# Kernel optimization log

Hardware: AMD Instinct MI355X
Metric: run time of the kernel (lower is better)

The kernel has to match this reference:

```python
import jax, jax.numpy as jnp
import numpy as np

D_MODEL = 1024
N_HEADS = 16
D_K = 64
CHUNK_LEN = 64


def setup_inputs() -> dict:
    key = jax.random.key(0)
    ks = jax.random.split(key, 10)
    B, S = 4, 2048
    NC, NN, NL = 32, 2, 128
    s = 1.0 / np.sqrt(D_MODEL)
    inp = {
        "query": jax.random.normal(ks[0], (B, S, D_MODEL), dtype=jnp.float32),
        "key": jax.random.normal(ks[1], (B, NC, NN, NL, D_MODEL), dtype=jnp.float32),
        # Linear weights stored as [in, out] (equivalent to torch W.T)
        "Wq": jax.random.normal(ks[2], (D_MODEL, N_HEADS * D_K), dtype=jnp.float32) * s,
        "bq": jnp.zeros((N_HEADS * D_K,), dtype=jnp.float32),
        "Wk": jax.random.normal(ks[3], (D_MODEL, N_HEADS * D_K), dtype=jnp.float32) * s,
        "bk": jnp.zeros((N_HEADS * D_K,), dtype=jnp.float32),
        "Wv": jax.random.normal(ks[4], (D_MODEL, N_HEADS * D_K), dtype=jnp.float32) * s,
        "bv": jnp.zeros((N_HEADS * D_K,), dtype=jnp.float32),
        "Wo": jax.random.normal(ks[5], (N_HEADS * D_K, D_MODEL), dtype=jnp.float32) * s,
        "bo": jnp.zeros((D_MODEL,), dtype=jnp.float32),
    }
    return inp


def reference(query, key, Wq, bq, Wk, bk, Wv, bv, Wo, bo):
    B, S, D = query.shape
    _, NC, NN, NL, _ = key.shape
    L = NN * NL  # kv length per chunk
    # reshape query into chunks: [B, NC, chunk_len, D]
    q_in = query.reshape(B, NC, CHUNK_LEN, D)
    kv_in = key.reshape(B, NC, L, D)  # key used for both K and V in the original
    # projections, split heads: [B, NC, H, T, d_k]
    q = (q_in @ Wq + bq).reshape(B, NC, CHUNK_LEN, N_HEADS, D_K).transpose(0, 1, 3, 2, 4)
    k = (kv_in @ Wk + bk).reshape(B, NC, L, N_HEADS, D_K).transpose(0, 1, 3, 2, 4)
    v = (kv_in @ Wv + bv).reshape(B, NC, L, N_HEADS, D_K).transpose(0, 1, 3, 2, 4)
    # attention per (batch, chunk, head)
    scores = jnp.einsum("bchqd,bchkd->bchqk", q, k) / jnp.sqrt(jnp.float32(D_K))
    attn = jax.nn.softmax(scores, axis=-1)
    o = jnp.einsum("bchqk,bchkd->bchqd", attn, v)
    # merge heads: [B, NC, chunk_len, H*d_k]
    o = o.transpose(0, 1, 3, 2, 4).reshape(B, NC, CHUNK_LEN, N_HEADS * D_K)
    out = o @ Wo + bo
    return out.reshape(B, S, D)
```

## Files before the change

### kernel.cpp

```cpp
#include <hip/hip_runtime.h>
#include <hip/hip_bf16.h>
#include <stdint.h>

#define DMODEL 1024
#define NHEADS 16
#define DK 64
#define TQ 64
#define LKV 256
#define MQ 8192
#define MKV 32768

typedef __bf16 bf16x8 __attribute__((ext_vector_type(8)));
typedef float f32x4 __attribute__((ext_vector_type(4)));
typedef unsigned short u16x8 __attribute__((ext_vector_type(8)));
typedef unsigned short u16;

__device__ __forceinline__ unsigned short f2bf(float f) {
    union { float f; unsigned int i; } x; x.f = f;
    unsigned int r = (x.i + 0x7FFFu + ((x.i >> 16) & 1u)) >> 16;
    return (unsigned short)r;
}

__device__ __forceinline__ void gload_lds16(const void* g, void* l) {
    __builtin_amdgcn_global_load_lds(
        (const __attribute__((address_space(1))) unsigned int*)g,
        (__attribute__((address_space(3))) unsigned int*)l, 16, 0, 0);
}

__global__ __launch_bounds__(256) void cvt_f32_bf16(const float* __restrict__ in,
                                                    unsigned short* __restrict__ out) {
    long long i = ((long long)blockIdx.x * 256 + threadIdx.x) * 8;
    f32x4 a = *(const f32x4*)(in + i);
    f32x4 b = *(const f32x4*)(in + i + 4);
    u16x8 o;
    o[0] = f2bf(a[0]); o[1] = f2bf(a[1]); o[2] = f2bf(a[2]); o[3] = f2bf(a[3]);
    o[4] = f2bf(b[0]); o[5] = f2bf(b[1]); o[6] = f2bf(b[2]); o[7] = f2bf(b[3]);
    *(u16x8*)(out + i) = o;
}

__global__ __launch_bounds__(256) void transpose_w_cvt4(const float* __restrict__ w0,
                                                        const float* __restrict__ w1,
                                                        const float* __restrict__ w2,
                                                        const float* __restrict__ w3,
                                                        u16* __restrict__ o0,
                                                        u16* __restrict__ o1,
                                                        u16* __restrict__ o2,
                                                        u16* __restrict__ o3) {
    __shared__ float tile[64][65];
    const float* in; u16* out;
    switch (blockIdx.z) {
        case 0: in = w0; out = o0; break;
        case 1: in = w1; out = o1; break;
        case 2: in = w2; out = o2; break;
        default: in = w3; out = o3; break;
    }
    int bi = blockIdx.y, bj = blockIdx.x;
    int tid = threadIdx.x;
    int c = tid & 63, r0 = tid >> 6;
#pragma unroll
    for (int p = 0; p < 16; ++p) {
        int r = r0 + 4 * p;
        tile[r][c] = in[(size_t)(bi * 64 + r) * 1024 + bj * 64 + c];
    }
    __syncthreads();
#pragma unroll
    for (int p = 0; p < 16; ++p) {
        int r = r0 + 4 * p;
        out[(size_t)(bj * 64 + r) * 1024 + bi * 64 + c] = f2bf(tile[c][r]);
    }
}

template <int OUTMODE>
__global__ __launch_bounds__(256) void gemm_bias(const u16* __restrict__ A,
                                                 const u16* __restrict__ Bt,
                                                 const float* __restrict__ bias,
                                                 void* __restrict__ OutV) {
    __shared__ alignas(16) u16 aLds[128 * 32];
    __shared__ alignas(16) u16 bLds[128 * 32];

    int tid = threadIdx.x;
    int lane = tid & 63, wid = tid >> 6;
    int m0 = blockIdx.x * 128;
    int n0 = blockIdx.y * 128;
    int wr = (wid >> 1) * 64, wc = (wid & 1) * 64;

    f32x4 zero = {0.f, 0.f, 0.f, 0.f};
    f32x4 acc[4][4];
#pragma unroll
    for (int i = 0; i < 4; ++i)
#pragma unroll
        for (int j = 0; j < 4; ++j) acc[i][j] = zero;

    int sr = lane >> 2;
    int sk = (lane & 3) * 8;
    const u16* aG = A + (size_t)(m0 + sr) * 1024 + sk;
    const u16* bG = Bt + (size_t)(n0 + sr) * 1024 + sk;
    int c0 = wid, c1 = wid + 4;

    int fr = lane & 15, fg = (lane >> 4) * 8;

    for (int kt = 0; kt < 1024; kt += 32) {
        gload_lds16(aG + (size_t)(c0 * 16) * 1024 + kt, aLds + c0 * 512);
        gload_lds16(aG + (size_t)(c1 * 16) * 1024 + kt, aLds + c1 * 512);
        gload_lds16(bG + (size_t)(c0 * 16) * 1024 + kt, bLds + c0 * 512);
        gload_lds16(bG + (size_t)(c1 * 16) * 1024 + kt, bLds + c1 * 512);
        __syncthreads();

        bf16x8 af[4], bf[4];
#pragma unroll
        for (int mt = 0; mt < 4; ++mt)
            af[mt] = *(const bf16x8*)&aLds[(wr + mt * 16 + fr) * 32 + fg];
#pragma unroll
        for (int nt = 0; nt < 4; ++nt)
            bf[nt] = *(const bf16x8*)&bLds[(wc + nt * 16 + fr) * 32 + fg];
#pragma unroll
        for (int mt = 0; mt < 4; ++mt)
#pragma unroll
            for (int nt = 0; nt < 4; ++nt)
                acc[mt][nt] = __builtin_amdgcn_mfma_f32_16x16x32_bf16(af[mt], bf[nt], acc[mt][nt], 0, 0, 0);
        __syncthreads();
    }

    float bv[4];
#pragma unroll
    for (int nt = 0; nt < 4; ++nt) bv[nt] = bias[n0 + wc + nt * 16 + fr];

    if (OUTMODE == 0) {
        u16* Out = (u16*)OutV;
#pragma unroll
        for (int mt = 0; mt < 4; ++mt)
#pragma unroll
            for (int r = 0; r < 4; ++r) {
                size_t row = (size_t)(m0 + wr + mt * 16 + (lane >> 4) * 4 + r);
#pragma unroll
                for (int nt = 0; nt < 4; ++nt)
                    Out[row * 1024 + n0 + wc + nt * 16 + fr] = f2bf(acc[mt][nt][r] + bv[nt]);
            }
    } else {
        float* Out = (float*)OutV;
#pragma unroll
        for (int mt = 0; mt < 4; ++mt)
#pragma unroll
            for (int r = 0; r < 4; ++r) {
                size_t row = (size_t)(m0 + wr + mt * 16 + (lane >> 4) * 4 + r);
#pragma unroll
                for (int nt = 0; nt < 4; ++nt)
                    Out[row * 1024 + n0 + wc + nt * 16 + fr] = acc[mt][nt][r] + bv[nt];
            }
    }
}


__device__ __forceinline__ void stageA64(const u16* src, u16* ldsTile, int row0, int tid) {
    int w = tid >> 6, l = tid & 63;
    int r = row0 + w * 8 + (l >> 3);
    int k16 = (l & 7) ^ ((l >> 3) & 7);
    gload_lds16(src + (size_t)r * 1024 + k16 * 8, ldsTile + (size_t)(row0 + w * 8) * 64);
}
__device__ __forceinline__ void stageB64(const u16* src, u16* ldsTile, int j, int odd, int tid) {
    int w = tid >> 6, l = tid & 63;
    int ib = j * 64 + w * 8;
    int rowbase = ((ib >> 5) << 6) + (ib & 31) + (odd ? 32 : 0);
    int r = rowbase + (l >> 3);
    int k16 = (l & 7) ^ ((l >> 3) & 7);
    gload_lds16(src + (size_t)r * 1024 + k16 * 8, ldsTile + (size_t)rowbase * 64);
}

#define VMWAIT2() asm volatile("s_waitcnt vmcnt(2)" ::: "memory")
#define VMWAIT0() asm volatile("s_waitcnt vmcnt(0)" ::: "memory")
#define SBAR()    do { __builtin_amdgcn_s_barrier(); asm volatile("" ::: "memory"); } while (0)

__global__ __launch_bounds__(512, 2) void proj_fused(const u16* __restrict__ Akv,
                                                     const u16* __restrict__ Aq,
                                                     const u16* __restrict__ WkT,
                                                     const u16* __restrict__ WvT,
                                                     const u16* __restrict__ WqT,
                                                     const float* __restrict__ bk,
                                                     const float* __restrict__ bv,
                                                     const float* __restrict__ bq,
                                                     u16* __restrict__ Kp,
                                                     u16* __restrict__ Vt,
                                                     u16* __restrict__ Qp,
                                                     int nmKV, int nmQ) {
    __shared__ alignas(16) u16 lds[65536];
    u16* ldsA0 = lds;          u16* ldsA1 = lds + 16384;
    u16* ldsB0 = lds + 32768;  u16* ldsB1 = lds + 49152;

    int tid = threadIdx.x, lane = tid & 63, wid = tid >> 6;
    int wm = wid >> 2, wn = wid & 3;

    int nB = gridDim.x;
    int bid = blockIdx.x;
    int qq = nB >> 3, rr = nB & 7;
    int xcd = bid & 7, idx = bid >> 3;
    int wg = (xcd < rr) ? xcd * (qq + 1) + idx : rr * (qq + 1) + (xcd - rr) * qq + idx;

    const u16* A; const u16* B; const float* bias; u16* Out; int mode;
    int nKV4 = nmKV * 4;
    int lwg;
    if (wg < nKV4)            { lwg = wg;            A = Akv; B = WkT; bias = bk; Out = Kp; mode = 0; }
    else if (wg < 2 * nKV4)   { lwg = wg - nKV4;     A = Akv; B = WvT; bias = bv; Out = Vt; mode = 1; }
    else                      { lwg = wg - 2 * nKV4; A = Aq;  B = WqT; bias = bq; Out = Qp; mode = 0; }
    int m0 = (lwg >> 2) * 256;
    int n0 = (lwg & 3) * 256;

    const u16* aSrc = A + (size_t)m0 * 1024;
    const u16* bSrc = B + (size_t)n0 * 1024;

    f32x4 zero = {0.f, 0.f, 0.f, 0.f};
    f32x4 acc[8][4];
#pragma unroll
    for (int i = 0; i < 8; ++i)
#pragma unroll
        for (int j = 0; j < 4; ++j) acc[i][j] = zero;

    bf16x8 aR[4][2], b0R[2][2], b1R[2][2];

#define READ_A(lA, half)                                                         \
    do {                                                                         \
        _Pragma("unroll") for (int mf = 0; mf < 4; ++mf) {                       \
            int row = wm * 128 + (half) * 64 + mf * 16 + (lane & 15);            \
            _Pragma("unroll") for (int kk = 0; kk < 2; ++kk) {                   \
                int k16 = kk * 4 + (lane >> 4);                                  \
                aR[mf][kk] = *(const bf16x8*)&(lA)[row * 64 + ((k16 ^ (row & 7)) << 3)]; \
            }                                                                    \
        }                                                                        \
    } while (0)
#define READ_B(lB, half, dst)                                                    \
    do {                                                                         \
        _Pragma("unroll") for (int nf = 0; nf < 2; ++nf) {                       \
            int row = wn * 64 + (half) * 32 + nf * 16 + (lane & 15);             \
            _Pragma("unroll") for (int kk = 0; kk < 2; ++kk) {                   \
                int k16 = kk * 4 + (lane >> 4);                                  \
                dst[nf][kk] = *(const bf16x8*)&(lB)[row * 64 + ((k16 ^ (row & 7)) << 3)]; \
            }                                                                    \
        }                                                                        \
    } while (0)
#define MFMA16(mh, nh, bR)                                                       \
    do {                                                                         \
        __builtin_amdgcn_s_setprio(1);                                           \
        _Pragma("unroll") for (int mf = 0; mf < 4; ++mf)                         \
            _Pragma("unroll") for (int nf = 0; nf < 2; ++nf)                     \
                _Pragma("unroll") for (int kk = 0; kk < 2; ++kk)                 \
                    acc[(mh)*4 + mf][(nh)*2 + nf] =                              \
                        __builtin_amdgcn_mfma_f32_16x16x32_bf16(                 \
                            aR[mf][kk], bR[nf][kk], acc[(mh)*4 + mf][(nh)*2 + nf], 0, 0, 0); \
        __builtin_amdgcn_s_setprio(0);                                           \
    } while (0)

    stageA64(aSrc, ldsA0, 0, tid);    stageA64(aSrc, ldsA0, 128, tid);
    stageB64(bSrc, ldsB0, 0, 0, tid); stageB64(bSrc, ldsB0, 1, 0, tid);
    stageB64(bSrc, ldsB0, 0, 1, tid); stageB64(bSrc, ldsB0, 1, 1, tid);
    stageA64(aSrc, ldsA0, 64, tid);   stageA64(aSrc, ldsA0, 192, tid);
    VMWAIT0();
    SBAR();

    for (int t = 0; t < 16; ++t) {
        int cur = t & 1;
        u16* lA = cur ? ldsA1 : ldsA0;
        u16* lB = cur ? ldsB1 : ldsB0;
        u16* pA = cur ? ldsA0 : ldsA1;
        u16* pB = cur ? ldsB0 : ldsB1;
        const u16* aNext = aSrc + (t + 1) * 64;
        const u16* bNext = bSrc + (t + 1) * 64;
        bool pf = (t < 15);

        VMWAIT2();
        READ_A(lA, 0);
        READ_B(lB, 0, b0R);
        if (pf) { stageA64(aNext, pA, 0, tid); stageA64(aNext, pA, 128, tid); }
        SBAR();
        MFMA16(0, 0, b0R);
        SBAR();

        if (pf) { VMWAIT2(); } else { VMWAIT0(); }
        READ_B(lB, 1, b1R);
        if (pf) { stageB64(bNext, pB, 0, 0, tid); stageB64(bNext, pB, 1, 0, tid); }
        SBAR();
        MFMA16(0, 1, b1R);
        SBAR();

        READ_A(lA, 1);
        if (pf) { stageB64(bNext, pB, 0, 1, tid); stageB64(bNext, pB, 1, 1, tid); }
        SBAR();
        MFMA16(1, 1, b1R);
        SBAR();

        if (pf) {
            VMWAIT2();
            stageA64(aNext, pA, 64, tid); stageA64(aNext, pA, 192, tid);
        }
        SBAR();
        MFMA16(1, 0, b0R);
        SBAR();
    }

    float bvv[4];
#pragma unroll
    for (int NF = 0; NF < 4; ++NF) bvv[NF] = bias[n0 + wn * 64 + NF * 16 + (lane & 15)];

    if (mode == 0) {
#pragma unroll
        for (int MF = 0; MF < 8; ++MF)
#pragma unroll
            for (int r = 0; r < 4; ++r) {
                size_t row = (size_t)(m0 + wm * 128 + MF * 16 + (lane >> 4) * 4 + r);
#pragma unroll
                for (int NF = 0; NF < 4; ++NF)
                    Out[row * 1024 + n0 + wn * 64 + NF * 16 + (lane & 15)] =
                        f2bf(acc[MF][NF][r] + bvv[NF]);
            }
    } else {
#pragma unroll
        for (int MF = 0; MF < 8; ++MF)
#pragma unroll
            for (int r = 0; r < 4; ++r) {
                int gm = m0 + wm * 128 + MF * 16 + (lane >> 4) * 4 + r;
                int bc2 = gm >> 8, lv = gm & 255;
#pragma unroll
                for (int NF = 0; NF < 4; ++NF) {
                    int n = n0 + wn * 64 + NF * 16 + (lane & 15);
                    int hh = n >> 6, dd = n & 63;
                    Out[(size_t)((bc2 * 16 + hh) * 64 + dd) * 256 + lv] =
                        f2bf(acc[MF][NF][r] + bvv[NF]);
                }
            }
    }
#undef READ_A
#undef READ_B
#undef MFMA16
}

__global__ __launch_bounds__(256) void attn_kernel(const u16* __restrict__ Q,
                                                   const u16* __restrict__ K,
                                                   const u16* __restrict__ Vt,
                                                   u16* O) {
    __shared__ alignas(16) u16 pLds[64 * 264];

    int tid = threadIdx.x;
    int lane = tid & 63, w = tid >> 6;
    int bc = blockIdx.x >> 4, h = blockIdx.x & 15;
    int fr = lane & 15, g = lane >> 4;

    const u16* qb = Q + (size_t)(bc * 64 + w * 16 + fr) * 1024 + h * 64 + g * 8;
    bf16x8 qf0 = *(const bf16x8*)qb;
    bf16x8 qf1 = *(const bf16x8*)(qb + 32);

    const u16* kb = K + (size_t)(bc * 256 + fr) * 1024 + h * 64 + g * 8;

    f32x4 zero = {0.f, 0.f, 0.f, 0.f};
    f32x4 sc[16];
#pragma unroll
    for (int nt = 0; nt < 16; ++nt) sc[nt] = zero;

#pragma unroll
    for (int nt = 0; nt < 16; ++nt) {
        bf16x8 kf0 = *(const bf16x8*)(kb + (size_t)(nt * 16) * 1024);
        bf16x8 kf1 = *(const bf16x8*)(kb + (size_t)(nt * 16) * 1024 + 32);
        sc[nt] = __builtin_amdgcn_mfma_f32_16x16x32_bf16(qf0, kf0, sc[nt], 0, 0, 0);
        sc[nt] = __builtin_amdgcn_mfma_f32_16x16x32_bf16(qf1, kf1, sc[nt], 0, 0, 0);
    }

    const float scale = 0.125f;
    float mx[4], sum[4];
#pragma unroll
    for (int r = 0; r < 4; ++r) {
        float m = -1e30f;
#pragma unroll
        for (int nt = 0; nt < 16; ++nt) {
            sc[nt][r] *= scale;
            m = fmaxf(m, sc[nt][r]);
        }
#pragma unroll
        for (int x = 1; x < 16; x <<= 1) m = fmaxf(m, __shfl_xor(m, x, 64));
        mx[r] = m;
        sum[r] = 0.f;
    }
#pragma unroll
    for (int nt = 0; nt < 16; ++nt)
#pragma unroll
        for (int r = 0; r < 4; ++r) {
            float p = __expf(sc[nt][r] - mx[r]);
            sum[r] += p;
            pLds[(w * 16 + g * 4 + r) * 264 + nt * 16 + fr] = f2bf(p);
        }
#pragma unroll
    for (int r = 0; r < 4; ++r)
#pragma unroll
        for (int x = 1; x < 16; x <<= 1) sum[r] += __shfl_xor(sum[r], x, 64);

    __syncthreads();

    f32x4 oa[4];
#pragma unroll
    for (int nt = 0; nt < 4; ++nt) oa[nt] = zero;

    const u16* vtb = Vt + (size_t)((bc * 16 + h) * 64) * 256;
#pragma unroll
    for (int ks = 0; ks < 8; ++ks) {
        bf16x8 pf = *(const bf16x8*)&pLds[(w * 16 + fr) * 264 + ks * 32 + g * 8];
#pragma unroll
        for (int nt = 0; nt < 4; ++nt) {
            bf16x8 vf = *(const bf16x8*)(vtb + (size_t)(nt * 16 + fr) * 256 + ks * 32 + g * 8);
            oa[nt] = __builtin_amdgcn_mfma_f32_16x16x32_bf16(pf, vf, oa[nt], 0, 0, 0);
        }
    }

    float rs[4];
#pragma unroll
    for (int r = 0; r < 4; ++r) rs[r] = 1.0f / sum[r];

    u16* ob = O + (size_t)(bc * 64 + w * 16 + g * 4) * 1024 + h * 64 + fr;
#pragma unroll
    for (int nt = 0; nt < 4; ++nt)
#pragma unroll
        for (int r = 0; r < 4; ++r)
            ob[(size_t)r * 1024 + nt * 16] = f2bf(oa[nt][r] * rs[r]);
}

extern "C" void kernel_launch(void* const* d_in, const int* in_sizes, int n_in,
                              void* d_out, int out_size, void* d_ws, size_t ws_size,
                              hipStream_t stream) {
    const float* query = (const float*)d_in[0];
    const float* keyin = (const float*)d_in[1];
    const float* Wq = (const float*)d_in[2];
    const float* bq = (const float*)d_in[3];
    const float* Wk = (const float*)d_in[4];
    const float* bk = (const float*)d_in[5];
    const float* Wv = (const float*)d_in[6];
    const float* bv = (const float*)d_in[7];
    const float* Wo = (const float*)d_in[8];
    const float* bo = (const float*)d_in[9];

    u16* ws = (u16*)d_ws;
    const size_t MB1 = 1024 * 1024;

    u16* WqT = ws;
    u16* WkT = ws + MB1;
    u16* WvT = ws + 2 * MB1;
    u16* WoT = ws + 3 * MB1;
    u16* qb16 = ws + 4 * MB1;
    u16* Qp   = qb16 + (size_t)MQ * 1024;
    u16* kvb  = Qp + (size_t)MQ * 1024;

    size_t ws_elems = ws_size / 2;
    size_t fixed = 4 * MB1 + 2 * (size_t)MQ * 1024;
    size_t avail = (ws_elems > fixed) ? (ws_elems - fixed) : 0;
    long long max_rows = (long long)(avail / (3 * 1024));
    int slice_rows = (int)((max_rows / 256) * 256);
    if (slice_rows >= MKV) slice_rows = MKV;
    else if (slice_rows >= 16384) slice_rows = 16384;
    if (slice_rows < 256) slice_rows = 256;

    u16* Kp = kvb + (size_t)slice_rows * 1024;
    u16* Vt = Kp + (size_t)slice_rows * 1024;

    dim3 tb(256);
    transpose_w_cvt4<<<dim3(16, 16, 4), tb, 0, stream>>>(Wq, Wk, Wv, Wo, WqT, WkT, WvT, WoT);
    cvt_f32_bf16<<<dim3(MQ * 1024 / (256 * 8)), tb, 0, stream>>>(query, qb16);

    for (int r0 = 0; r0 < MKV; r0 += slice_rows) {
        int rows = MKV - r0;
        if (rows > slice_rows) rows = slice_rows;
        cvt_f32_bf16<<<dim3(rows * 1024 / (256 * 8)), tb, 0, stream>>>(
            keyin + (size_t)r0 * 1024, kvb);
        int nmKV = rows / 256;
        int nmQ = (r0 == 0) ? (MQ / 256) : 0;
        proj_fused<<<dim3(nmKV * 8 + nmQ * 4), dim3(512), 0, stream>>>(
            kvb, qb16, WkT, WvT, WqT, bk, bv, bq, Kp, Vt, Qp, nmKV, nmQ);
        size_t qoff = (size_t)(r0 / 4) * 1024;
        attn_kernel<<<dim3((rows / 256) * 16), tb, 0, stream>>>(
            Qp + qoff, Kp, Vt, Qp + qoff);
    }

    gemm_bias<2><<<dim3(MQ / 128, 8), tb, 0, stream>>>(Qp, WoT, bo, d_out);
}
```

Before: 322.0 us.

## Prefetch projection GEMM tiles two k-steps ahead with batched async loads

The projection GEMM main loop used to interleave the global-to-LDS loads for the next k-tile across the four MFMA phases. It now issues whole 8-load batches two tiles ahead, using the two LDS buffers as a ring, and retunes the vmcnt waits to match. The aim is to hide more global-memory latency behind MFMA work and to remove waits inside the loop. In exchange it keeps more loads in flight, and the hand-counted vmcnt values must stay exactly in step with the load order.

```diff
diff --git a/kernel.cpp b/kernel.cpp
--- a/kernel.cpp
+++ b/kernel.cpp
@@ -166,9 +166,19 @@
     gload_lds16(src + (size_t)r * 1024 + k16 * 8, ldsTile + (size_t)rowbase * 64);
 }
 
-#define VMWAIT2() asm volatile("s_waitcnt vmcnt(2)" ::: "memory")
-#define VMWAIT0() asm volatile("s_waitcnt vmcnt(0)" ::: "memory")
-#define SBAR()    do { __builtin_amdgcn_s_barrier(); asm volatile("" ::: "memory"); } while (0)
+#define SBAR() do { __builtin_amdgcn_s_barrier(); asm volatile("" ::: "memory"); } while (0)
+
+__device__ __forceinline__ void issueBatch(const u16* aT, const u16* bT,
+                                           u16* ldsA, u16* ldsB, int tid) {
+    stageA64(aT, ldsA, 0, tid);
+    stageA64(aT, ldsA, 128, tid);
+    stageB64(bT, ldsB, 0, 0, tid);
+    stageB64(bT, ldsB, 1, 0, tid);
+    stageB64(bT, ldsB, 0, 1, tid);
+    stageB64(bT, ldsB, 1, 1, tid);
+    stageA64(aT, ldsA, 64, tid);
+    stageA64(aT, ldsA, 192, tid);
+}
 
 __global__ __launch_bounds__(512, 2) void proj_fused(const u16* __restrict__ Akv,
                                                      const u16* __restrict__ Aq,
@@ -248,47 +258,39 @@
         __builtin_amdgcn_s_setprio(0);                                           \
     } while (0)
 
-    stageA64(aSrc, ldsA0, 0, tid);    stageA64(aSrc, ldsA0, 128, tid);
-    stageB64(bSrc, ldsB0, 0, 0, tid); stageB64(bSrc, ldsB0, 1, 0, tid);
-    stageB64(bSrc, ldsB0, 0, 1, tid); stageB64(bSrc, ldsB0, 1, 1, tid);
-    stageA64(aSrc, ldsA0, 64, tid);   stageA64(aSrc, ldsA0, 192, tid);
-    VMWAIT0();
+    issueBatch(aSrc, bSrc, ldsA0, ldsB0, tid);
+    issueBatch(aSrc + 64, bSrc + 64, ldsA1, ldsB1, tid);
+    asm volatile("s_waitcnt vmcnt(8)" ::: "memory");
     SBAR();
 
     for (int t = 0; t < 16; ++t) {
         int cur = t & 1;
         u16* lA = cur ? ldsA1 : ldsA0;
         u16* lB = cur ? ldsB1 : ldsB0;
-        u16* pA = cur ? ldsA0 : ldsA1;
-        u16* pB = cur ? ldsB0 : ldsB1;
-        const u16* aNext = aSrc + (t + 1) * 64;
-        const u16* bNext = bSrc + (t + 1) * 64;
-        bool pf = (t < 15);
-
-        VMWAIT2();
+
+        if (t < 15) { asm volatile("s_waitcnt vmcnt(10)" ::: "memory"); }
+        else        { asm volatile("s_waitcnt vmcnt(2)" ::: "memory"); }
         READ_A(lA, 0);
         READ_B(lB, 0, b0R);
-        if (pf) { stageA64(aNext, pA, 0, tid); stageA64(aNext, pA, 128, tid); }
         SBAR();
         MFMA16(0, 0, b0R);
         SBAR();
 
-        if (pf) { VMWAIT2(); } else { VMWAIT0(); }
+        if (t < 15) { asm volatile("s_waitcnt vmcnt(8)" ::: "memory"); }
+        else        { asm volatile("s_waitcnt vmcnt(0)" ::: "memory"); }
         READ_B(lB, 1, b1R);
-        if (pf) { stageB64(bNext, pB, 0, 0, tid); stageB64(bNext, pB, 1, 0, tid); }
         SBAR();
         MFMA16(0, 1, b1R);
         SBAR();
 
         READ_A(lA, 1);
-        if (pf) { stageB64(bNext, pB, 0, 1, tid); stageB64(bNext, pB, 1, 1, tid); }
         SBAR();
         MFMA16(1, 1, b1R);
         SBAR();
 
-        if (pf) {
-            VMWAIT2();
-            stageA64(aNext, pA, 64, tid); stageA64(aNext, pA, 192, tid);
+        asm volatile("s_waitcnt vmcnt(4)" ::: "memory");
+        if (t < 14) {
+            issueBatch(aSrc + (t + 2) * 64, bSrc + (t + 2) * 64, lA, lB, tid);
         }
         SBAR();
         MFMA16(1, 0, b0R);
```

Measured after the change: 334.8 us. 1.04x slower.
